# Kernel optimization log

Hardware: AMD Instinct MI355X
Metric: run time of the kernel (lower is better)

Reference implementation:

```python
import jax, jax.numpy as jnp
import numpy as np

STRIDE, PAD, DIL = 1, 1, 1


def setup_inputs() -> dict:
    key = jax.random.key(0)
    ks = jax.random.split(key, 5)
    N, Cin, H, W = 8, 256, 56, 56
    Cout, kh, kw = 256, 3, 3
    x = jax.random.normal(ks[0], (N, Cin, H, W), jnp.float32)
    offset = jax.random.normal(ks[1], (N, 2 * kh * kw, H, W), jnp.float32)
    mask = jax.random.uniform(ks[2], (N, kh * kw, H, W), jnp.float32)
    fan_in = Cin * kh * kw
    bound = float(np.sqrt(6.0 / fan_in))  # kaiming_uniform, relu gain
    weight = jax.random.uniform(ks[3], (Cout, Cin, kh, kw), jnp.float32, -bound, bound)
    bias = jnp.zeros((Cout,), jnp.float32)
    return {"x": x, "offset": offset, "mask": mask, "weight": weight, "bias": bias}


def _mdcn(x, offset, mask, weight, bias):
    N, Cin, H, W = x.shape
    Cout, _, kh, kw = weight.shape
    K = kh * kw
    Hout = (H + 2 * PAD - (DIL * (kh - 1) + 1)) // STRIDE + 1
    Wout = (W + 2 * PAD - (DIL * (kw - 1) + 1)) // STRIDE + 1
    # offset channels: [K, 2(y,x)] interleaved -> [N,K,2,Hout,Wout]
    off = offset.reshape(N, K, 2, Hout, Wout)
    dy, dx = off[:, :, 0], off[:, :, 1]
    ky = (jnp.arange(K) // kw) * DIL
    kx = (jnp.arange(K) % kw) * DIL
    base_y = jnp.arange(Hout) * STRIDE - PAD
    base_x = jnp.arange(Wout) * STRIDE - PAD
    py = dy + ky[None, :, None, None] + base_y[None, None, :, None]  # [N,K,Ho,Wo]
    px = dx + kx[None, :, None, None] + base_x[None, None, None, :]
    y0 = jnp.floor(py)
    x0 = jnp.floor(px)
    wy1 = py - y0
    wx1 = px - x0
    wy0 = 1.0 - wy1
    wx0 = 1.0 - wx1
    y0i = y0.astype(jnp.int32)
    x0i = x0.astype(jnp.int32)
    x_nhwc = jnp.transpose(x, (0, 2, 3, 1))  # [N,H,W,Cin]
    nidx = jnp.arange(N)[:, None, None, None]

    def gather(yi, xi):
        valid = (yi >= 0) & (yi < H) & (xi >= 0) & (xi < W)
        yc = jnp.clip(yi, 0, H - 1)
        xc = jnp.clip(xi, 0, W - 1)
        v = x_nhwc[nidx, yc, xc]  # [N,K,Ho,Wo,Cin]
        return v * valid[..., None].astype(x.dtype)

    v = (gather(y0i, x0i) * (wy0 * wx0)[..., None]
         + gather(y0i, x0i + 1) * (wy0 * wx1)[..., None]
         + gather(y0i + 1, x0i) * (wy1 * wx0)[..., None]
         + gather(y0i + 1, x0i + 1) * (wy1 * wx1)[..., None])
    v = v * mask.reshape(N, K, Hout, Wout)[..., None]
    wr = weight.reshape(Cout, Cin, K)
    out = jnp.einsum('nkhwc,ock->nohw', v, wr)
    return out + bias[None, :, None, None]


def reference(x, offset, mask, weight, bias):
    return _mdcn(x, offset, mask, weight, bias)
```

## Files before the change

### kernel.cpp

```cpp
#include <hip/hip_runtime.h>
#include <math.h>

#define H_ 56
#define W_ 56
#define CIN 256
#define COUT 256
#define NB 8
#define SPIX 3136
#define KG 2304
#define MTOT 25088
#define MT 128
#define NBLK 196
#define GUARD_PX 2048

typedef __bf16 v8bf __attribute__((ext_vector_type(8)));
typedef float  v4f  __attribute__((ext_vector_type(4)));

#define WAIT_VM(N)  do { asm volatile("s_waitcnt vmcnt(" #N ")" ::: "memory"); \
                         __builtin_amdgcn_sched_barrier(0); } while (0)
#define WAIT_LGKM0  do { asm volatile("s_waitcnt lgkmcnt(0)" ::: "memory"); \
                         __builtin_amdgcn_sched_barrier(0); } while (0)
#define BARR        do { asm volatile("s_barrier" ::: "memory"); } while (0)

__device__ __forceinline__ void async_copy16(const void* g, void* l) {
    __builtin_amdgcn_global_load_lds(
        (const __attribute__((address_space(1))) void*)g,
        (__attribute__((address_space(3))) void*)l, 16, 0, 0);
}

__global__ __launch_bounds__(256) void prep_xw(const float* __restrict__ x,
                                               const float* __restrict__ w,
                                               __bf16* __restrict__ xb,
                                               __bf16* __restrict__ bp) {
    __shared__ float tile[64][65];
    const int tid = threadIdx.x;
    if (blockIdx.z < 8) {
        const int n = blockIdx.z, c0 = blockIdx.y * 64, s0 = blockIdx.x * 64;
        const float* xp = x + (size_t)n * CIN * SPIX;
        __bf16* xo = xb + (size_t)n * SPIX * CIN;
#pragma unroll
        for (int i = 0; i < 16; ++i) {
            int idx = tid + i * 256;
            int cr = idx >> 6, sc = idx & 63;
            tile[cr][sc] = xp[(c0 + cr) * SPIX + s0 + sc];
        }
        __syncthreads();
#pragma unroll
        for (int i = 0; i < 16; ++i) {
            int idx = tid + i * 256;
            int sr = idx >> 6, cc = idx & 63;
            xo[(s0 + sr) * CIN + c0 + cc] = (__bf16)tile[cc][sr];
        }
    } else {
        const int base = (blockIdx.y * 49 + blockIdx.x) * 256 + tid;
        for (int i = base; i < COUT * KG; i += 196 * 256) {
            const int o = i / KG;
            const int rem = i - o * KG;
            const int c = rem / 9;
            const int tap = rem - c * 9;
            bp[(size_t)o * KG + tap * 256 + c] = (__bf16)w[i];
        }
    }
}

__device__ __forceinline__ void compute_params(
    const float* __restrict__ offs, const float* __restrict__ msk,
    int m0, int* sS, float4* sW, int tid)
{
    for (int idx = tid; idx < 9 * MT; idx += 512) {
        const int tl = idx >> 7, pl = idx & 127;
        const int pg = m0 + pl;
        const int n  = pg / SPIX;
        const int s  = pg - n * SPIX;
        const int h  = s / W_, w = s - h * W_;
        const int kY = tl / 3, kX = tl - kY * 3;
        const float dy = offs[n * (18 * SPIX) + (2 * tl) * SPIX + s];
        const float dx = offs[n * (18 * SPIX) + (2 * tl + 1) * SPIX + s];
        const float mk = msk[n * (9 * SPIX) + tl * SPIX + s];
        const float py = dy + (float)(kY + h - 1);
        const float px = dx + (float)(kX + w - 1);
        const float fy0 = floorf(py), fx0 = floorf(px);
        const int y0 = (int)fy0, x0 = (int)fx0;
        const float wy1 = py - fy0, wx1 = px - fx0;
        const float wy0 = 1.f - wy1, wx0 = 1.f - wx1;
        const bool yv0 = (y0 >= 0) & (y0 < H_);
        const bool yv1 = (y0 + 1 >= 0) & (y0 + 1 < H_);
        const bool xv0 = (x0 >= 0) & (x0 < W_);
        const bool xv1 = (x0 + 1 >= 0) & (x0 + 1 < W_);
        float4 wt;
        wt.x = (yv0 & xv0) ? wy0 * wx0 * mk : 0.f;
        wt.y = (yv0 & xv1) ? wy0 * wx1 * mk : 0.f;
        wt.z = (yv1 & xv0) ? wy1 * wx0 * mk : 0.f;
        wt.w = (yv1 & xv1) ? wy1 * wx1 * mk : 0.f;
        int base = n * SPIX + y0 * W_ + x0;
        base = min(max(base, -GUARD_PX), NB * SPIX - 58 + GUARD_PX);
        sS[idx] = base * CIN;
        sW[idx] = wt;
    }
}

__global__ __launch_bounds__(512, 2) void mdcn_fused4(
    const __bf16* __restrict__ xb,
    const float*  __restrict__ offs,
    const float*  __restrict__ msk,
    const __bf16* __restrict__ bp,
    const float*  __restrict__ bias,
    float*        __restrict__ out)
{
    __shared__ __align__(16) char smem[121344];
    int*    sS = (int*)(smem + 98304);
    float4* sW = (float4*)(smem + 102912);

    const int tid  = threadIdx.x;
    const int lane = tid & 63, wv = tid >> 6;
    const int wm = wv & 1, wn = wv >> 1;
    const int l15 = lane & 15, q = lane >> 4;

    const int xcd = blockIdx.x & 7, ib = blockIdx.x >> 3;
    const int wg  = (xcd < 4) ? xcd * 25 + ib : 100 + (xcd - 4) * 24 + ib;
    const int m0  = wg * MT;

    compute_params(offs, msk, m0, sS, sW, tid);

    v4f acc[4][4];
#pragma unroll
    for (int i = 0; i < 4; ++i)
#pragma unroll
        for (int j = 0; j < 4; ++j) acc[i][j] = (v4f)0.f;

    __syncthreads();

    const int pxl = tid >> 2, c2 = tid & 3;
    v8bf ga0, ga1, ga2, ga3, gb0, gb1, gb2, gb3;
    float4 cw;

#define GATHER(E, KQ)                                                   \
    { const int b_ = sS[E] + ((KQ) << 6) + c2 * 8;                      \
      cw  = sW[E];                                                      \
      ga0 = *(const v8bf*)(xb + b_);                                    \
      ga1 = *(const v8bf*)(xb + b_ + 256);                              \
      ga2 = *(const v8bf*)(xb + b_ + 14336);                            \
      ga3 = *(const v8bf*)(xb + b_ + 14592);                            \
      gb0 = *(const v8bf*)(xb + b_ + 32);                               \
      gb1 = *(const v8bf*)(xb + b_ + 288);                              \
      gb2 = *(const v8bf*)(xb + b_ + 14368);                            \
      gb3 = *(const v8bf*)(xb + b_ + 14624); }

#define COMBINE_STORE(AP)                                               \
    { v8bf r0, r1;                                                      \
      _Pragma("unroll")                                                 \
      for (int j = 0; j < 8; ++j) {                                     \
        r0[j] = (__bf16)(cw.x * (float)ga0[j] + cw.y * (float)ga1[j]    \
                       + cw.z * (float)ga2[j] + cw.w * (float)ga3[j]);  \
        r1[j] = (__bf16)(cw.x * (float)gb0[j] + cw.y * (float)gb1[j]    \
                       + cw.z * (float)gb2[j] + cw.w * (float)gb3[j]);  \
      }                                                                 \
      *(v8bf*)((AP) + pxl * 64 + (((c2)     ^ (pxl & 7)) << 3)) = r0;   \
      *(v8bf*)((AP) + pxl * 64 + (((c2 + 4) ^ (pxl & 7)) << 3)) = r1; }

#define STAGE_B(K0, LB)                                                 \
    { _Pragma("unroll")                                                 \
      for (int t = 0; t < 4; ++t) {                                     \
        const int brow = t * 64 + (wv << 3) + (lane >> 3);              \
        const int blc  = (lane & 7) ^ (brow & 7);                       \
        async_copy16(bp + (size_t)brow * KG + (K0) + blc * 8,           \
                     (LB) + ((t * 8 + wv) << 10)); }

    GATHER(pxl, 0)
    COMBINE_STORE((__bf16*)smem)
    STAGE_B(0, smem + 32768) }
    GATHER(pxl, 1)
    WAIT_LGKM0;
    WAIT_VM(8);
    BARR;

    char* ac = smem;          char* an = smem + 16384;
    char* bc = smem + 32768;  char* bn = smem + 65536;

#pragma unroll 1
    for (int ks = 0; ks < 36; ++ks) {
        if (ks < 35) {
            STAGE_B((ks + 1) << 6, bn) }
            WAIT_VM(4);
            COMBINE_STORE((__bf16*)an)
            if (ks < 34) {
                const int st = ks + 2;
                GATHER((st >> 2) * MT + pxl, st & 3)
            }
        }

        __builtin_amdgcn_s_setprio(1);
#pragma unroll
        for (int kf = 0; kf < 2; ++kf) {
            v8bf afr[4], bfr[4];
#pragma unroll
            for (int mt = 0; mt < 4; ++mt) {
                const int row = wm * 64 + mt * 16 + l15;
                const int pch = (kf * 4 + q) ^ (row & 7);
                afr[mt] = *(const v8bf*)((__bf16*)ac + row * 64 + pch * 8);
            }
#pragma unroll
            for (int nt = 0; nt < 4; ++nt) {
                const int row = wn * 64 + nt * 16 + l15;
                const int pch = (kf * 4 + q) ^ (row & 7);
                bfr[nt] = *(const v8bf*)((__bf16*)bc + row * 64 + pch * 8);
            }
#pragma unroll
            for (int mt = 0; mt < 4; ++mt)
#pragma unroll
                for (int nt = 0; nt < 4; ++nt)
                    acc[mt][nt] = __builtin_amdgcn_mfma_f32_16x16x32_bf16(
                        afr[mt], bfr[nt], acc[mt][nt], 0, 0, 0);
        }
        __builtin_amdgcn_s_setprio(0);

        if (ks < 34) {
            WAIT_LGKM0;
            WAIT_VM(8);
            BARR;
        } else if (ks == 34) {
            WAIT_LGKM0;
            WAIT_VM(0);
            BARR;
        }
        char* t;
        t = ac; ac = an; an = t;
        t = bc; bc = bn; bn = t;
    }
#undef GATHER
#undef COMBINE_STORE
#undef STAGE_B

    WAIT_LGKM0;
    BARR;
    float* epi = (float*)smem + wv * 1104;
    const int pg_l = m0 + wm * 64 + lane;
    const int n_l  = pg_l / SPIX;
    float* outp = out + (size_t)n_l * (COUT * SPIX) + (pg_l - n_l * SPIX);

#pragma unroll
    for (int nt = 0; nt < 4; ++nt) {
        const float bv = bias[wn * 64 + nt * 16 + l15];
#pragma unroll
        for (int mt = 0; mt < 4; ++mt)
#pragma unroll
            for (int r = 0; r < 4; ++r)
                epi[(mt * 16 + q * 4 + r) * 17 + l15] = acc[mt][nt][r] + bv;
#pragma unroll
        for (int oc = 0; oc < 16; ++oc)
            outp[(size_t)(wn * 64 + nt * 16 + oc) * SPIX] = epi[lane * 17 + oc];
    }
}

#define BM 64
#define BN 64
#define BKF 32
#define AST 68
#define BST 68
#define CST 65
__global__ __launch_bounds__(256) void mdcn_fallback(
    const float* __restrict__ xs, const float* __restrict__ offs,
    const float* __restrict__ msk, const float* __restrict__ wraw,
    const float* __restrict__ bias, float* __restrict__ out)
{
    __shared__ float smem[BKF * AST + BKF * BST];
    __shared__ int   sBase[4][BM];
    __shared__ float sWgt[4][BM];
    float (*At)[AST] = (float (*)[AST])smem;
    float (*Bt)[BST] = (float (*)[BST])(smem + BKF * AST);
    float (*Cs)[CST] = (float (*)[CST])smem;
    const int tid = threadIdx.x;
    const int m0 = blockIdx.x * BM;
    const int o0 = blockIdx.y * BN;
    const int n  = m0 / SPIX;
    const int s0 = m0 - n * SPIX;
    const int tx = tid & 15, ty = tid >> 4;
    float acc[4][4] = {};
    for (int k = 0; k < 9; ++k) {
        if (tid < BM) {
            const int s = s0 + tid;
            const int h = s / W_;
            const int w = s - h * W_;
            const int kY = k / 3, kX = k - kY * 3;
            const float dy = offs[(size_t)n * (18 * SPIX) + (size_t)(2 * k) * SPIX + s];
            const float dx = offs[(size_t)n * (18 * SPIX) + (size_t)(2 * k + 1) * SPIX + s];
            const float mk = msk[(size_t)n * (9 * SPIX) + (size_t)k * SPIX + s];
            const float py = dy + (float)(kY + h - 1);
            const float px = dx + (float)(kX + w - 1);
            const float fy0 = floorf(py), fx0 = floorf(px);
            const int y0 = (int)fy0, x0 = (int)fx0;
            const float wy1 = py - fy0, wx1 = px - fx0;
            const float wy0 = 1.0f - wy1, wx0 = 1.0f - wx1;
#pragma unroll
            for (int t = 0; t < 4; ++t) {
                const int yi = y0 + (t >> 1), xi = x0 + (t & 1);
                const bool valid = (yi >= 0) & (yi < H_) & (xi >= 0) & (xi < W_);
                const int yc = min(max(yi, 0), H_ - 1);
                const int xc = min(max(xi, 0), W_ - 1);
                float wt = ((t >> 1) ? wy1 : wy0) * ((t & 1) ? wx1 : wx0) * mk;
                sBase[t][tid] = n * (CIN * SPIX) + yc * W_ + xc;
                sWgt[t][tid] = valid ? wt : 0.0f;
            }
        }
        __syncthreads();
        for (int c0 = 0; c0 < CIN; c0 += BKF) {
#pragma unroll
            for (int i = 0; i < 8; ++i) {
                int idx = tid + i * 256;
                int row = idx >> 5, cc = idx & 31;
                int ce = (c0 + cc) * SPIX;
                At[cc][row] = sWgt[0][row] * xs[sBase[0][row] + ce]
                            + sWgt[1][row] * xs[sBase[1][row] + ce]
                            + sWgt[2][row] * xs[sBase[2][row] + ce]
                            + sWgt[3][row] * xs[sBase[3][row] + ce];
            }
#pragma unroll
            for (int i = 0; i < 8; ++i) {
                int idx = tid + i * 256;
                int kf = idx >> 6, o = idx & 63;
                Bt[kf][o] = wraw[(size_t)(o0 + o) * KG + (c0 + kf) * 9 + k];
            }
            __syncthreads();
#pragma unroll
            for (int kf = 0; kf < BKF; ++kf) {
                const float4 a = *(const float4*)&At[kf][ty * 4];
                const float4 b = *(const float4*)&Bt[kf][tx * 4];
                acc[0][0] = fmaf(a.x, b.x, acc[0][0]); acc[0][1] = fmaf(a.x, b.y, acc[0][1]);
                acc[0][2] = fmaf(a.x, b.z, acc[0][2]); acc[0][3] = fmaf(a.x, b.w, acc[0][3]);
                acc[1][0] = fmaf(a.y, b.x, acc[1][0]); acc[1][1] = fmaf(a.y, b.y, acc[1][1]);
                acc[1][2] = fmaf(a.y, b.z, acc[1][2]); acc[1][3] = fmaf(a.y, b.w, acc[1][3]);
                acc[2][0] = fmaf(a.z, b.x, acc[2][0]); acc[2][1] = fmaf(a.z, b.y, acc[2][1]);
                acc[2][2] = fmaf(a.z, b.z, acc[2][2]); acc[2][3] = fmaf(a.z, b.w, acc[2][3]);
                acc[3][0] = fmaf(a.w, b.x, acc[3][0]); acc[3][1] = fmaf(a.w, b.y, acc[3][1]);
                acc[3][2] = fmaf(a.w, b.z, acc[3][2]); acc[3][3] = fmaf(a.w, b.w, acc[3][3]);
            }
            __syncthreads();
        }
    }
#pragma unroll
    for (int i = 0; i < 4; ++i)
#pragma unroll
        for (int j = 0; j < 4; ++j)
            Cs[ty * 4 + i][tx * 4 + j] = acc[i][j] + bias[o0 + tx * 4 + j];
    __syncthreads();
    const int pix = tid & 63, ob = tid >> 6;
    float* outp = out + (size_t)n * COUT * SPIX + s0 + pix;
#pragma unroll
    for (int r = 0; r < 16; ++r) {
        int o = r * 4 + ob;
        outp[(size_t)(o0 + o) * SPIX] = Cs[pix][o];
    }
}

extern "C" void kernel_launch(void* const* d_in, const int* in_sizes, int n_in,
                              void* d_out, int out_size, void* d_ws, size_t ws_size,
                              hipStream_t stream) {
    const float* x    = (const float*)d_in[0];
    const float* offs = (const float*)d_in[1];
    const float* msk  = (const float*)d_in[2];
    const float* w    = (const float*)d_in[3];
    const float* bias = (const float*)d_in[4];
    float* out = (float*)d_out;

    const size_t GUARD_B  = (size_t)GUARD_PX * CIN * sizeof(__bf16);
    const size_t xb_bytes = (size_t)NB * SPIX * CIN * sizeof(__bf16);
    const size_t bp_bytes = (size_t)KG * COUT * sizeof(__bf16);
    const size_t need     = GUARD_B + xb_bytes + GUARD_B + bp_bytes;

    if (ws_size >= need) {
        __bf16* xb = (__bf16*)((char*)d_ws + GUARD_B);
        __bf16* bp = (__bf16*)((char*)d_ws + GUARD_B + xb_bytes + GUARD_B);
        hipMemsetAsync(d_ws, 0, GUARD_B, stream);
        hipMemsetAsync((char*)d_ws + GUARD_B + xb_bytes, 0, GUARD_B, stream);
        prep_xw<<<dim3(49, 4, 9), 256, 0, stream>>>(x, w, xb, bp);
        mdcn_fused4<<<dim3(NBLK), 512, 0, stream>>>(xb, offs, msk, bp, bias, out);
    } else {
        mdcn_fallback<<<dim3(MTOT / BM, COUT / BN), 256, 0, stream>>>(
            x, offs, msk, w, bias, out);
    }
}
```

Measured before the change: 156.0 us.

## Switch to fp16 with packed bilinear combine, fragment prefetch, fused guard zeroing

Changes the staged activations and weights from bf16 to fp16 so the bilinear combine can use packed half-precision vector multiply-adds instead of per-element float conversions, and uses f16 MFMA. Hoists LDS fragment loads for both k-halves ahead of the gather/stage work so they overlap with it. Replaces the two hipMemsetAsync calls for guard zones with an extra z-slice in the prep kernel. Doing the combine in fp16 loses some precision and fp16 range is narrower than bf16, and holding all fragments at once raises register pressure.

```diff
diff --git a/kernel.cpp b/kernel.cpp
--- a/kernel.cpp
+++ b/kernel.cpp
@@ -13,8 +13,8 @@
 #define NBLK 196
 #define GUARD_PX 2048
 
-typedef __bf16 v8bf __attribute__((ext_vector_type(8)));
-typedef float  v4f  __attribute__((ext_vector_type(4)));
+typedef _Float16 v8hf __attribute__((ext_vector_type(8)));
+typedef float    v4f  __attribute__((ext_vector_type(4)));
 
 #define WAIT_VM(N)  do { asm volatile("s_waitcnt vmcnt(" #N ")" ::: "memory"); \
                          __builtin_amdgcn_sched_barrier(0); } while (0)
@@ -30,14 +30,14 @@
 
 __global__ __launch_bounds__(256) void prep_xw(const float* __restrict__ x,
                                                const float* __restrict__ w,
-                                               __bf16* __restrict__ xb,
-                                               __bf16* __restrict__ bp) {
+                                               _Float16* __restrict__ xb,
+                                               _Float16* __restrict__ bp) {
     __shared__ float tile[64][65];
     const int tid = threadIdx.x;
     if (blockIdx.z < 8) {
         const int n = blockIdx.z, c0 = blockIdx.y * 64, s0 = blockIdx.x * 64;
         const float* xp = x + (size_t)n * CIN * SPIX;
-        __bf16* xo = xb + (size_t)n * SPIX * CIN;
+        _Float16* xo = xb + (size_t)n * SPIX * CIN;
 #pragma unroll
         for (int i = 0; i < 16; ++i) {
             int idx = tid + i * 256;
@@ -49,16 +49,25 @@
         for (int i = 0; i < 16; ++i) {
             int idx = tid + i * 256;
             int sr = idx >> 6, cc = idx & 63;
-            xo[(s0 + sr) * CIN + c0 + cc] = (__bf16)tile[cc][sr];
-        }
-    } else {
+            xo[(s0 + sr) * CIN + c0 + cc] = (_Float16)tile[cc][sr];
+        }
+    } else if (blockIdx.z == 8) {
         const int base = (blockIdx.y * 49 + blockIdx.x) * 256 + tid;
         for (int i = base; i < COUT * KG; i += 196 * 256) {
             const int o = i / KG;
             const int rem = i - o * KG;
             const int c = rem / 9;
             const int tap = rem - c * 9;
-            bp[(size_t)o * KG + tap * 256 + c] = (__bf16)w[i];
+            bp[(size_t)o * KG + tap * 256 + c] = (_Float16)w[i];
+        }
+    } else {
+        const int gtid = (blockIdx.y * 49 + blockIdx.x) * 256 + tid;
+        v8hf* lo = (v8hf*)(xb - (size_t)GUARD_PX * CIN);
+        v8hf* hi = (v8hf*)(xb + (size_t)NB * SPIX * CIN);
+        const v8hf z = (v8hf)(_Float16)0.f;
+        for (int i = gtid; i < 65536; i += 196 * 256) {
+            lo[i] = z;
+            hi[i] = z;
         }
     }
 }
@@ -99,13 +108,13 @@
     }
 }
 
-__global__ __launch_bounds__(512, 2) void mdcn_fused4(
-    const __bf16* __restrict__ xb,
-    const float*  __restrict__ offs,
-    const float*  __restrict__ msk,
-    const __bf16* __restrict__ bp,
-    const float*  __restrict__ bias,
-    float*        __restrict__ out)
+__global__ __launch_bounds__(512, 2) void mdcn_fused6(
+    const _Float16* __restrict__ xb,
+    const float*    __restrict__ offs,
+    const float*    __restrict__ msk,
+    const _Float16* __restrict__ bp,
+    const float*    __restrict__ bias,
+    float*          __restrict__ out)
 {
     __shared__ __align__(16) char smem[121344];
     int*    sS = (int*)(smem + 98304);
@@ -131,44 +140,67 @@
     __syncthreads();
 
     const int pxl = tid >> 2, c2 = tid & 3;
-    v8bf ga0, ga1, ga2, ga3, gb0, gb1, gb2, gb3;
+    v8hf ga0, ga1, ga2, ga3, gb0, gb1, gb2, gb3;
     float4 cw;
+    v8hf afr[2][4], bfr[2][4];
 
 #define GATHER(E, KQ)                                                   \
     { const int b_ = sS[E] + ((KQ) << 6) + c2 * 8;                      \
       cw  = sW[E];                                                      \
-      ga0 = *(const v8bf*)(xb + b_);                                    \
-      ga1 = *(const v8bf*)(xb + b_ + 256);                              \
-      ga2 = *(const v8bf*)(xb + b_ + 14336);                            \
-      ga3 = *(const v8bf*)(xb + b_ + 14592);                            \
-      gb0 = *(const v8bf*)(xb + b_ + 32);                               \
-      gb1 = *(const v8bf*)(xb + b_ + 288);                              \
-      gb2 = *(const v8bf*)(xb + b_ + 14368);                            \
-      gb3 = *(const v8bf*)(xb + b_ + 14624); }
+      ga0 = *(const v8hf*)(xb + b_);                                    \
+      ga1 = *(const v8hf*)(xb + b_ + 256);                              \
+      ga2 = *(const v8hf*)(xb + b_ + 14336);                            \
+      ga3 = *(const v8hf*)(xb + b_ + 14592);                            \
+      gb0 = *(const v8hf*)(xb + b_ + 32);                               \
+      gb1 = *(const v8hf*)(xb + b_ + 288);                              \
+      gb2 = *(const v8hf*)(xb + b_ + 14368);                            \
+      gb3 = *(const v8hf*)(xb + b_ + 14624); }
 
 #define COMBINE_STORE(AP)                                               \
-    { v8bf r0, r1;                                                      \
-      _Pragma("unroll")                                                 \
-      for (int j = 0; j < 8; ++j) {                                     \
-        r0[j] = (__bf16)(cw.x * (float)ga0[j] + cw.y * (float)ga1[j]    \
-                       + cw.z * (float)ga2[j] + cw.w * (float)ga3[j]);  \
-        r1[j] = (__bf16)(cw.x * (float)gb0[j] + cw.y * (float)gb1[j]    \
-                       + cw.z * (float)gb2[j] + cw.w * (float)gb3[j]);  \
-      }                                                                 \
-      *(v8bf*)((AP) + pxl * 64 + (((c2)     ^ (pxl & 7)) << 3)) = r0;   \
-      *(v8bf*)((AP) + pxl * 64 + (((c2 + 4) ^ (pxl & 7)) << 3)) = r1; }
+    { const _Float16 wx_ = (_Float16)cw.x, wy_ = (_Float16)cw.y;        \
+      const _Float16 wz_ = (_Float16)cw.z, ww_ = (_Float16)cw.w;        \
+      v8hf r0_ = ga0 * wx_ + ga1 * wy_ + ga2 * wz_ + ga3 * ww_;         \
+      v8hf r1_ = gb0 * wx_ + gb1 * wy_ + gb2 * wz_ + gb3 * ww_;         \
+      *(v8hf*)((AP) + pxl * 64 + (((c2)     ^ (pxl & 7)) << 3)) = r0_;  \
+      *(v8hf*)((AP) + pxl * 64 + (((c2 + 4) ^ (pxl & 7)) << 3)) = r1_; }
 
 #define STAGE_B(K0, LB)                                                 \
-    { _Pragma("unroll")                                                 \
+    do { _Pragma("unroll")                                              \
       for (int t = 0; t < 4; ++t) {                                     \
         const int brow = t * 64 + (wv << 3) + (lane >> 3);              \
         const int blc  = (lane & 7) ^ (brow & 7);                       \
         async_copy16(bp + (size_t)brow * KG + (K0) + blc * 8,           \
-                     (LB) + ((t * 8 + wv) << 10)); }
+                     (LB) + ((t * 8 + wv) << 10)); } } while (0)
+
+#define LOAD_FRAGS(AB, BB)                                              \
+    { _Pragma("unroll")                                                 \
+      for (int kf = 0; kf < 2; ++kf) {                                  \
+        _Pragma("unroll")                                               \
+        for (int mt = 0; mt < 4; ++mt) {                                \
+          const int row = wm * 64 + mt * 16 + l15;                      \
+          const int pch = (kf * 4 + q) ^ (row & 7);                     \
+          afr[kf][mt] = *(const v8hf*)((_Float16*)(AB) + row * 64 + pch * 8); } \
+        _Pragma("unroll")                                               \
+        for (int nt = 0; nt < 4; ++nt) {                                \
+          const int row = wn * 64 + nt * 16 + l15;                      \
+          const int pch = (kf * 4 + q) ^ (row & 7);                     \
+          bfr[kf][nt] = *(const v8hf*)((_Float16*)(BB) + row * 64 + pch * 8); } } }
+
+#define MFMA_EXEC                                                       \
+    { __builtin_amdgcn_s_setprio(1);                                    \
+      _Pragma("unroll")                                                 \
+      for (int kf = 0; kf < 2; ++kf)                                    \
+        _Pragma("unroll")                                               \
+        for (int mt = 0; mt < 4; ++mt)                                  \
+          _Pragma("unroll")                                             \
+          for (int nt = 0; nt < 4; ++nt)                                \
+            acc[mt][nt] = __builtin_amdgcn_mfma_f32_16x16x32_f16(       \
+                afr[kf][mt], bfr[kf][nt], acc[mt][nt], 0, 0, 0);        \
+      __builtin_amdgcn_s_setprio(0); }
 
     GATHER(pxl, 0)
-    COMBINE_STORE((__bf16*)smem)
-    STAGE_B(0, smem + 32768) }
+    COMBINE_STORE((_Float16*)smem)
+    STAGE_B(0, smem + 32768);
     GATHER(pxl, 1)
     WAIT_LGKM0;
     WAIT_VM(8);
@@ -179,40 +211,18 @@
 
 #pragma unroll 1
     for (int ks = 0; ks < 36; ++ks) {
+        LOAD_FRAGS(ac, bc);
         if (ks < 35) {
-            STAGE_B((ks + 1) << 6, bn) }
+            STAGE_B((ks + 1) << 6, bn);
             WAIT_VM(4);
-            COMBINE_STORE((__bf16*)an)
+            COMBINE_STORE((_Float16*)an)
             if (ks < 34) {
                 const int st = ks + 2;
                 GATHER((st >> 2) * MT + pxl, st & 3)
             }
         }
 
-        __builtin_amdgcn_s_setprio(1);
-#pragma unroll
-        for (int kf = 0; kf < 2; ++kf) {
-            v8bf afr[4], bfr[4];
-#pragma unroll
-            for (int mt = 0; mt < 4; ++mt) {
-                const int row = wm * 64 + mt * 16 + l15;
-                const int pch = (kf * 4 + q) ^ (row & 7);
-                afr[mt] = *(const v8bf*)((__bf16*)ac + row * 64 + pch * 8);
-            }
-#pragma unroll
-            for (int nt = 0; nt < 4; ++nt) {
-                const int row = wn * 64 + nt * 16 + l15;
-                const int pch = (kf * 4 + q) ^ (row & 7);
-                bfr[nt] = *(const v8bf*)((__bf16*)bc + row * 64 + pch * 8);
-            }
-#pragma unroll
-            for (int mt = 0; mt < 4; ++mt)
-#pragma unroll
-                for (int nt = 0; nt < 4; ++nt)
-                    acc[mt][nt] = __builtin_amdgcn_mfma_f32_16x16x32_bf16(
-                        afr[mt], bfr[nt], acc[mt][nt], 0, 0, 0);
-        }
-        __builtin_amdgcn_s_setprio(0);
+        MFMA_EXEC;
 
         if (ks < 34) {
             WAIT_LGKM0;
@@ -230,6 +240,8 @@
 #undef GATHER
 #undef COMBINE_STORE
 #undef STAGE_B
+#undef LOAD_FRAGS
+#undef MFMA_EXEC
 
     WAIT_LGKM0;
     BARR;
@@ -362,18 +374,16 @@
     const float* bias = (const float*)d_in[4];
     float* out = (float*)d_out;
 
-    const size_t GUARD_B  = (size_t)GUARD_PX * CIN * sizeof(__bf16);
-    const size_t xb_bytes = (size_t)NB * SPIX * CIN * sizeof(__bf16);
-    const size_t bp_bytes = (size_t)KG * COUT * sizeof(__bf16);
+    const size_t GUARD_B  = (size_t)GUARD_PX * CIN * sizeof(_Float16);
+    const size_t xb_bytes = (size_t)NB * SPIX * CIN * sizeof(_Float16);
+    const size_t bp_bytes = (size_t)KG * COUT * sizeof(_Float16);
     const size_t need     = GUARD_B + xb_bytes + GUARD_B + bp_bytes;
 
     if (ws_size >= need) {
-        __bf16* xb = (__bf16*)((char*)d_ws + GUARD_B);
-        __bf16* bp = (__bf16*)((char*)d_ws + GUARD_B + xb_bytes + GUARD_B);
-        hipMemsetAsync(d_ws, 0, GUARD_B, stream);
-        hipMemsetAsync((char*)d_ws + GUARD_B + xb_bytes, 0, GUARD_B, stream);
-        prep_xw<<<dim3(49, 4, 9), 256, 0, stream>>>(x, w, xb, bp);
-        mdcn_fused4<<<dim3(NBLK), 512, 0, stream>>>(xb, offs, msk, bp, bias, out);
+        _Float16* xb = (_Float16*)((char*)d_ws + GUARD_B);
+        _Float16* bp = (_Float16*)((char*)d_ws + GUARD_B + xb_bytes + GUARD_B);
+        prep_xw<<<dim3(49, 4, 10), 256, 0, stream>>>(x, w, xb, bp);
+        mdcn_fused6<<<dim3(NBLK), 512, 0, stream>>>(xb, offs, msk, bp, bias, out);
     } else {
         mdcn_fallback<<<dim3(MTOT / BM, COUT / BN), 256, 0, stream>>>(
             x, offs, msk, w, bias, out);
```

New measurement: 143.3 us, median of 2. 1.09x faster.
